# Kernel tuning notes

Measured on AMD Instinct MI355X. Metric: run time of the kernel, lower is better.

The kernel has to match this reference:

```python
import jax, jax.numpy as jnp
import numpy as np

SIGMA = 1.0
EPSILON = 1.0
MAX_ITER = 10


def pairwise_kernel(x, y, sigma=SIGMA):
    # k = -||x-y||^2 / (2 sigma^2), shape [B, L, K]
    outer = jnp.einsum('bld,bkd->blk', x, y)
    nx = jnp.sum(x * x, axis=2)
    ny = jnp.sum(y * y, axis=2)
    dist = jnp.clip(nx[:, :, None] + ny[:, None, :] - 2.0 * outer, 0.0, None)
    return -dist / (2.0 * sigma ** 2)


def c_transform(potential, log_weight, kernel, epsilon=EPSILON):
    # rho=None => scale=1, lse = -eps * logsumexp(kernel/eps + (pot/eps + log_w))
    s = potential / epsilon + log_weight            # [B, K]
    operand = kernel / epsilon + s[:, None, :]      # [B, L, K]
    return -epsilon * jax.scipy.special.logsumexp(operand, axis=2)


def potentials(kxy, log_a, log_b):
    kyx = jnp.swapaxes(kxy, 1, 2)
    f0 = jnp.zeros_like(log_a)
    g0 = jnp.zeros_like(log_b)

    def step(carry, _):
        f, g = carry
        fn = c_transform(g, log_b, kxy)
        gn = c_transform(f, log_a, kyx)
        return ((fn + f) * 0.5, (gn + g) * 0.5), None

    (f, g), _ = jax.lax.scan(step, (f0, g0), None, length=MAX_ITER)
    return f, g


def sym_potential(x, log_a):
    kxx = pairwise_kernel(x, x)
    f0 = jnp.zeros_like(log_a)

    def step(f, _):
        fn = c_transform(f, log_a, kxx)
        return (fn + f) * 0.5, None

    f, _ = jax.lax.scan(step, f0, None, length=MAX_ITER)
    return f


def evaluate_potential(x, a, y, b, g):
    # phi_transform is identity for rho=None; scaled_dot_prod forward = sum(a*f, dim=1)
    kxy = pairwise_kernel(x, y)
    f = c_transform(g, jnp.log(b), kxy)
    return jnp.sum(a * f, axis=1)


def setup_inputs() -> dict:
    key = jax.random.key(0)
    k1, k2, k3, k4 = jax.random.split(key, 4)
    B, L, K, D = 8, 2048, 2048, 32
    x = jax.random.normal(k1, (B, L, D), dtype=jnp.float32)
    y = jax.random.normal(k2, (B, K, D), dtype=jnp.float32)
    a = jax.random.uniform(k3, (B, L), dtype=jnp.float32, minval=0.1, maxval=1.0)
    b = jax.random.uniform(k4, (B, K), dtype=jnp.float32, minval=0.1, maxval=1.0)
    a = a / jnp.sum(a, axis=1, keepdims=True)
    b = b / jnp.sum(b, axis=1, keepdims=True)
    return {"x": x, "a": a, "y": y, "b": b}


def reference(x, a, y, b):
    log_a, log_b = jnp.log(a), jnp.log(b)
    kxy = pairwise_kernel(x, y)
    f, g = potentials(kxy, log_a, log_b)
    dist = evaluate_potential(x, a, y, b, g) + evaluate_potential(y, b, x, a, f)
    fx = sym_potential(x, log_a)
    fy = sym_potential(y, log_b)
    ent_x = evaluate_potential(x, a, x, a, fx)
    ent_y = evaluate_potential(y, b, y, b, fy)
    return jnp.mean(dist - ent_x - ent_y)
```

## Files before the change

### kernel.cpp

```cpp
#include <hip/hip_runtime.h>
#include <math.h>

#define BATCH 8
#define NPT   2048
#define DIM   32
#define RPB   64
#define CPW   (NPT / 4)
#define NT    (CPW / 16)
#define L2E   1.44269504088896f
#define BIAS2   96.0f
#define BIASLN  66.54212933375474f
#define BN    (BATCH * NPT)

typedef __attribute__((ext_vector_type(8))) _Float16 half8;
typedef __attribute__((ext_vector_type(4))) float floatx4;
typedef unsigned short u16;
typedef unsigned int u32;

__device__ __forceinline__ u16 f2h_bits(float v) {
    _Float16 h = (_Float16)v;
    return *(u16*)&h;
}
__device__ __forceinline__ float exp2v(float x) { return __builtin_amdgcn_exp2f(x); }

struct CtSet {
    const u16* Ah;
    const u16* Bh;
    const float* tls;
    const float* qX;
    const float* normR;
    const float* cn;
    const float* bmIn;
    const float* cwNext;
    const float* prev;
    float* out;
    float* tlsOut;
    float* bmOut;
};
struct CtArgs { CtSet s[4]; int average; };

__global__ __launch_bounds__(256, 4) void ct_kernel(CtArgs args) {
    const CtSet cs = args.s[blockIdx.y];
    const int batch = blockIdx.z;
    const int row0 = blockIdx.x * RPB;
    const int tid  = threadIdx.x;
    const int w = tid >> 6, lane = tid & 63, n = lane & 15, quad = lane >> 4;
    const int qk = quad * 8;
    const size_t pbase = (size_t)batch * NPT * DIM;
    const size_t vbase = (size_t)batch * NPT;

    __shared__ float lsum[RPB][4];

    const u16* __restrict__ Ah = cs.Ah + pbase;
    const u16* __restrict__ Bh = cs.Bh + pbase;
    const float* __restrict__ tls = cs.tls + vbase;

    half8 ah[4];
    #pragma unroll
    for (int s = 0; s < 4; s++) {
        size_t off = (size_t)(row0 + s * 16 + n) * DIM + qk;
        ah[s] = *(const half8*)(Ah + off);
    }

    float tmv = fmaxf(cs.bmIn[batch * 128 + lane], cs.bmIn[batch * 128 + 64 + lane]);
    #pragma unroll
    for (int m = 1; m < 64; m <<= 1) tmv = fmaxf(tmv, __shfl_xor(tmv, m, 64));
    const float Tmax = tmv;
    const float cnv = cs.cn[batch];

    float M0s[4][4];
    #pragma unroll
    for (int s = 0; s < 4; s++)
        #pragma unroll
        for (int r = 0; r < 4; r++) {
            int row = row0 + s * 16 + quad * 4 + r;
            M0s[s][r] = L2E * (cs.normR[vbase + row] * cnv + Tmax) - BIAS2;
        }

    float sum[4][4];
    #pragma unroll
    for (int s = 0; s < 4; s++)
        #pragma unroll
        for (int r = 0; r < 4; r++) sum[s][r] = 0.0f;

    const int c0 = w * CPW + n;
    const u16* bp = Bh + (size_t)c0 * DIM + qk;
    const float* tp = tls + c0;

    half8 b0, b1;
    float t0, t1;
    b0 = *(const half8*)bp;  t0 = *tp;

    #pragma unroll 1
    for (int ch = 0; ch < NT; ch += 2) {
        b1 = *(const half8*)(bp + (size_t)(ch + 1) * 16 * DIM);
        t1 = tp[(ch + 1) * 16];
        {
            floatx4 acc[4];
            #pragma unroll
            for (int s = 0; s < 4; s++)
                acc[s] = (floatx4){t0 - M0s[s][0], t0 - M0s[s][1],
                                   t0 - M0s[s][2], t0 - M0s[s][3]};
            #pragma unroll
            for (int s = 0; s < 4; s++)
                acc[s] = __builtin_amdgcn_mfma_f32_16x16x32_f16(ah[s], b0, acc[s], 0, 0, 0);
            #pragma unroll
            for (int s = 0; s < 4; s++)
                #pragma unroll
                for (int r = 0; r < 4; r++)
                    sum[s][r] += exp2v(acc[s][r]);
        }
        if (ch + 2 < NT) {
            b0 = *(const half8*)(bp + (size_t)(ch + 2) * 16 * DIM);
            t0 = tp[(ch + 2) * 16];
        }
        {
            floatx4 acc[4];
            #pragma unroll
            for (int s = 0; s < 4; s++)
                acc[s] = (floatx4){t1 - M0s[s][0], t1 - M0s[s][1],
                                   t1 - M0s[s][2], t1 - M0s[s][3]};
            #pragma unroll
            for (int s = 0; s < 4; s++)
                acc[s] = __builtin_amdgcn_mfma_f32_16x16x32_f16(ah[s], b1, acc[s], 0, 0, 0);
            #pragma unroll
            for (int s = 0; s < 4; s++)
                #pragma unroll
                for (int r = 0; r < 4; r++)
                    sum[s][r] += exp2v(acc[s][r]);
        }
    }

    #pragma unroll
    for (int s = 0; s < 4; s++)
        #pragma unroll
        for (int r = 0; r < 4; r++) {
            float v = sum[s][r];
            #pragma unroll
            for (int m = 1; m < 16; m <<= 1) v += __shfl_xor(v, m, 64);
            if (n == 0) lsum[s * 16 + quad * 4 + r][w] = v;
        }
    __syncthreads();

    if (tid < RPB) {
        float T = (lsum[tid][0] + lsum[tid][1]) + (lsum[tid][2] + lsum[tid][3]);
        int l = row0 + tid;
        float M0 = cs.normR[vbase + l] * cnv + Tmax;
        float lse = M0 + __logf(T) - BIASLN;
        float val = cs.qX[vbase + l] - lse;
        if (args.average) val = 0.5f * (cs.prev[vbase + l] + val);
        cs.out[vbase + l] = val;
        float tc = val + cs.cwNext[vbase + l];
        cs.tlsOut[vbase + l] = L2E * tc;
        float bm = tc;
        #pragma unroll
        for (int m = 1; m < 16; m <<= 1) bm = fmaxf(bm, __shfl_xor(bm, m, 64));
        if ((tid & 15) == 0)
            cs.bmOut[batch * 128 + blockIdx.x * 4 + (tid >> 4)] = bm;
    }
}

struct InitArgs {
    const float *x, *a, *y, *b;
    float *c_x, *c_y, *qx, *qy, *nx, *ny;
    u16 *xh, *yh, *xsh, *ysh;
    float *f0, *g0, *fx0, *fy0;
    float *tlsF0, *tlsG0, *tlsFx0, *tlsFy0;
    float *bmF0, *bmG0, *bmFx0, *bmFy0;
};

__global__ __launch_bounds__(256) void init_kernel(InitArgs ia) {
    int idx = blockIdx.x * 256 + threadIdx.x;
    if (idx >= BN) return;
    const float* xp = ia.x + (size_t)idx * DIM;
    const float* yp = ia.y + (size_t)idx * DIM;
    u32* xhp  = (u32*)ia.xh  + (size_t)idx * (DIM / 2);
    u32* yhp  = (u32*)ia.yh  + (size_t)idx * (DIM / 2);
    u32* xshp = (u32*)ia.xsh + (size_t)idx * (DIM / 2);
    u32* yshp = (u32*)ia.ysh + (size_t)idx * (DIM / 2);
    float sx = 0.f, sy = 0.f;
    #pragma unroll
    for (int d = 0; d < DIM; d += 2) {
        float v0 = xp[d], v1 = xp[d + 1];
        sx += v0 * v0 + v1 * v1;
        xhp[d / 2]  = (u32)f2h_bits(v0) | ((u32)f2h_bits(v1) << 16);
        xshp[d / 2] = (u32)f2h_bits(L2E * v0) | ((u32)f2h_bits(L2E * v1) << 16);
        float u0 = yp[d], u1 = yp[d + 1];
        sy += u0 * u0 + u1 * u1;
        yhp[d / 2]  = (u32)f2h_bits(u0) | ((u32)f2h_bits(u1) << 16);
        yshp[d / 2] = (u32)f2h_bits(L2E * u0) | ((u32)f2h_bits(L2E * u1) << 16);
    }
    float qxv = 0.5f * sx, qyv = 0.5f * sy;
    ia.qx[idx] = qxv; ia.qy[idx] = qyv;
    ia.nx[idx] = sqrtf(sx); ia.ny[idx] = sqrtf(sy);
    float cxv = __logf(ia.a[idx]) - qxv;
    float cyv = __logf(ia.b[idx]) - qyv;
    ia.c_x[idx] = cxv; ia.c_y[idx] = cyv;
    ia.f0[idx] = 0.f; ia.g0[idx] = 0.f; ia.fx0[idx] = 0.f; ia.fy0[idx] = 0.f;
    ia.tlsF0[idx] = L2E * cxv; ia.tlsG0[idx] = L2E * cyv;
    ia.tlsFx0[idx] = L2E * cxv; ia.tlsFy0[idx] = L2E * cyv;
    float mx = cxv, my = cyv;
    #pragma unroll
    for (int m = 1; m < 16; m <<= 1) {
        mx = fmaxf(mx, __shfl_xor(mx, m, 32));
        my = fmaxf(my, __shfl_xor(my, m, 32));
    }
    if ((threadIdx.x & 15) == 0) {
        int g = idx >> 4;
        ia.bmF0[g] = mx; ia.bmFx0[g] = mx;
        ia.bmG0[g] = my; ia.bmFy0[g] = my;
    }
}

__global__ __launch_bounds__(256) void precomp_kernel(const float* __restrict__ qx,
                                                      const float* __restrict__ qy,
                                                      float* __restrict__ cn) {
    int side = blockIdx.x, batch = blockIdx.y;
    const float* q = side ? qy : qx;
    float m = 0.f;
    for (int k = threadIdx.x; k < NPT; k += 256) m = fmaxf(m, q[(size_t)batch * NPT + k]);
    #pragma unroll
    for (int mm = 1; mm < 64; mm <<= 1) m = fmaxf(m, __shfl_xor(m, mm, 64));
    __shared__ float sm[4];
    if ((threadIdx.x & 63) == 0) sm[threadIdx.x >> 6] = m;
    __syncthreads();
    if (threadIdx.x == 0) {
        float v = fmaxf(fmaxf(sm[0], sm[1]), fmaxf(sm[2], sm[3]));
        cn[side * BATCH + batch] = sqrtf(2.f * v);
    }
}

__global__ __launch_bounds__(1024) void reduce_kernel(
        const float* __restrict__ a, const float* __restrict__ b,
        const float* __restrict__ ctA, const float* __restrict__ ctB,
        const float* __restrict__ ctX, const float* __restrict__ ctY,
        float* __restrict__ out) {
    float acc = 0.f;
    for (int idx = threadIdx.x; idx < BN; idx += 1024) {
        acc += a[idx] * (ctA[idx] - ctX[idx]) + b[idx] * (ctB[idx] - ctY[idx]);
    }
    #pragma unroll
    for (int off = 32; off > 0; off >>= 1) acc += __shfl_down(acc, off, 64);
    __shared__ float sm[16];
    if ((threadIdx.x & 63) == 0) sm[threadIdx.x >> 6] = acc;
    __syncthreads();
    if (threadIdx.x == 0) {
        float t = 0.f;
        #pragma unroll
        for (int i = 0; i < 16; i++) t += sm[i];
        out[0] = t / (float)BATCH;
    }
}

extern "C" void kernel_launch(void* const* d_in, const int* in_sizes, int n_in,
                              void* d_out, int out_size, void* d_ws, size_t ws_size,
                              hipStream_t stream) {
    const float* x = (const float*)d_in[0];
    const float* a = (const float*)d_in[1];
    const float* y = (const float*)d_in[2];
    const float* b = (const float*)d_in[3];
    float* out = (float*)d_out;

    float* ws = (float*)d_ws;
    float* c_x = ws + 0 * BN;
    float* c_y = ws + 1 * BN;
    float* qx  = ws + 2 * BN;
    float* qy  = ws + 3 * BN;
    float* nx  = ws + 4 * BN;
    float* ny  = ws + 5 * BN;
    float* fb[2]  = { ws + 6 * BN,  ws + 7 * BN };
    float* gb[2]  = { ws + 8 * BN,  ws + 9 * BN };
    float* fxb[2] = { ws + 10 * BN, ws + 11 * BN };
    float* fyb[2] = { ws + 12 * BN, ws + 13 * BN };
    float* ctA = ws + 14 * BN;
    float* ctB = ws + 15 * BN;
    float* ctX = ws + 16 * BN;
    float* ctY = ws + 17 * BN;
    float* tlsF[2]  = { ws + 18 * BN, ws + 19 * BN };
    float* tlsG[2]  = { ws + 20 * BN, ws + 21 * BN };
    float* tlsFx[2] = { ws + 22 * BN, ws + 23 * BN };
    float* tlsFy[2] = { ws + 24 * BN, ws + 25 * BN };
    float* dummyT = ws + 26 * BN;
    float* small = ws + 27 * BN;
    float* bmF[2]  = { small + 0 * 1024, small + 1 * 1024 };
    float* bmG[2]  = { small + 2 * 1024, small + 3 * 1024 };
    float* bmFx[2] = { small + 4 * 1024, small + 5 * 1024 };
    float* bmFy[2] = { small + 6 * 1024, small + 7 * 1024 };
    float* dummyB = small + 8 * 1024;
    float* cn = small + 9 * 1024;
    u16* bf = (u16*)(small + 10 * 1024);
    const size_t AS = (size_t)BN * DIM;
    u16* xh  = bf + 0 * AS;
    u16* yh  = bf + 1 * AS;
    u16* xsh = bf + 2 * AS;
    u16* ysh = bf + 3 * AS;

    InitArgs ia;
    ia.x = x; ia.a = a; ia.y = y; ia.b = b;
    ia.c_x = c_x; ia.c_y = c_y; ia.qx = qx; ia.qy = qy; ia.nx = nx; ia.ny = ny;
    ia.xh = xh; ia.yh = yh; ia.xsh = xsh; ia.ysh = ysh;
    ia.f0 = fb[0]; ia.g0 = gb[0]; ia.fx0 = fxb[0]; ia.fy0 = fyb[0];
    ia.tlsF0 = tlsF[0]; ia.tlsG0 = tlsG[0]; ia.tlsFx0 = tlsFx[0]; ia.tlsFy0 = tlsFy[0];
    ia.bmF0 = bmF[0]; ia.bmG0 = bmG[0]; ia.bmFx0 = bmFx[0]; ia.bmFy0 = bmFy[0];
    init_kernel<<<BN / 256, 256, 0, stream>>>(ia);
    precomp_kernel<<<dim3(2, BATCH), 256, 0, stream>>>(qx, qy, cn);

    dim3 grid(NPT / RPB, 4, BATCH);
    int cur = 0;
    for (int it = 0; it < 10; it++) {
        CtArgs ar;
        ar.average = 1;
        ar.s[0] = { xh, ysh, tlsG[cur], qx, nx, cn + BATCH, bmG[cur], c_x,
                    fb[cur], fb[1 - cur], tlsF[1 - cur], bmF[1 - cur] };
        ar.s[1] = { yh, xsh, tlsF[cur], qy, ny, cn, bmF[cur], c_y,
                    gb[cur], gb[1 - cur], tlsG[1 - cur], bmG[1 - cur] };
        ar.s[2] = { xh, xsh, tlsFx[cur], qx, nx, cn, bmFx[cur], c_x,
                    fxb[cur], fxb[1 - cur], tlsFx[1 - cur], bmFx[1 - cur] };
        ar.s[3] = { yh, ysh, tlsFy[cur], qy, ny, cn + BATCH, bmFy[cur], c_y,
                    fyb[cur], fyb[1 - cur], tlsFy[1 - cur], bmFy[1 - cur] };
        ct_kernel<<<grid, 256, 0, stream>>>(ar);
        cur ^= 1;
    }

    CtArgs fin;
    fin.average = 0;
    fin.s[0] = { xh, ysh, tlsG[cur], qx, nx, cn + BATCH, bmG[cur], c_x,
                 fb[cur], ctA, dummyT, dummyB };
    fin.s[1] = { yh, xsh, tlsF[cur], qy, ny, cn, bmF[cur], c_y,
                 gb[cur], ctB, dummyT, dummyB };
    fin.s[2] = { xh, xsh, tlsFx[cur], qx, nx, cn, bmFx[cur], c_x,
                 fxb[cur], ctX, dummyT, dummyB };
    fin.s[3] = { yh, ysh, tlsFy[cur], qy, ny, cn + BATCH, bmFy[cur], c_y,
                 fyb[cur], ctY, dummyT, dummyB };
    ct_kernel<<<grid, 256, 0, stream>>>(fin);

    reduce_kernel<<<1, 1024, 0, stream>>>(a, b, ctA, ctB, ctX, ctY, out);
}
```

Before: 338.2 us.

## Factor column weight out of exp, drop per-row bias, halve rows per block

Rewrites the logsumexp stabilisation. The per-column term is now computed once as a weight exp2(t - Tmax) and applied with an FMA to exp2 of the raw MFMA dot product, replacing the per-row norm-based bias seeded into the accumulator. This removes the normR/cn inputs, the precompute kernel and the per-row bias subtraction. Rows per block drop from 64 to 32 and launch bounds rise to 8 blocks per CU, which halves A-fragment reuse per B load but allows more occupancy. The change risks overflow or underflow in exp2 of the unbiased dot product and in the separately exponentiated weight, since the per-row max shift is gone.

```diff
diff --git a/kernel.cpp b/kernel.cpp
--- a/kernel.cpp
+++ b/kernel.cpp
@@ -4,12 +4,10 @@
 #define BATCH 8
 #define NPT   2048
 #define DIM   32
-#define RPB   64
+#define RPB   32
 #define CPW   (NPT / 4)
 #define NT    (CPW / 16)
 #define L2E   1.44269504088896f
-#define BIAS2   96.0f
-#define BIASLN  66.54212933375474f
 #define BN    (BATCH * NPT)
 
 typedef __attribute__((ext_vector_type(8))) _Float16 half8;
@@ -28,8 +26,6 @@
     const u16* Bh;
     const float* tls;
     const float* qX;
-    const float* normR;
-    const float* cn;
     const float* bmIn;
     const float* cwNext;
     const float* prev;
@@ -39,7 +35,7 @@
 };
 struct CtArgs { CtSet s[4]; int average; };
 
-__global__ __launch_bounds__(256, 4) void ct_kernel(CtArgs args) {
+__global__ __launch_bounds__(256, 8) void ct_kernel(CtArgs args) {
     const CtSet cs = args.s[blockIdx.y];
     const int batch = blockIdx.z;
     const int row0 = blockIdx.x * RPB;
@@ -55,9 +51,9 @@
     const u16* __restrict__ Bh = cs.Bh + pbase;
     const float* __restrict__ tls = cs.tls + vbase;
 
-    half8 ah[4];
-    #pragma unroll
-    for (int s = 0; s < 4; s++) {
+    half8 ah[2];
+    #pragma unroll
+    for (int s = 0; s < 2; s++) {
         size_t off = (size_t)(row0 + s * 16 + n) * DIM + qk;
         ah[s] = *(const half8*)(Ah + off);
     }
@@ -66,20 +62,11 @@
     #pragma unroll
     for (int m = 1; m < 64; m <<= 1) tmv = fmaxf(tmv, __shfl_xor(tmv, m, 64));
     const float Tmax = tmv;
-    const float cnv = cs.cn[batch];
-
-    float M0s[4][4];
-    #pragma unroll
-    for (int s = 0; s < 4; s++)
-        #pragma unroll
-        for (int r = 0; r < 4; r++) {
-            int row = row0 + s * 16 + quad * 4 + r;
-            M0s[s][r] = L2E * (cs.normR[vbase + row] * cnv + Tmax) - BIAS2;
-        }
-
-    float sum[4][4];
-    #pragma unroll
-    for (int s = 0; s < 4; s++)
+    const float l2eTmax = L2E * Tmax;
+
+    float sum[2][4];
+    #pragma unroll
+    for (int s = 0; s < 2; s++)
         #pragma unroll
         for (int r = 0; r < 4; r++) sum[s][r] = 0.0f;
 
@@ -96,43 +83,41 @@
         b1 = *(const half8*)(bp + (size_t)(ch + 1) * 16 * DIM);
         t1 = tp[(ch + 1) * 16];
         {
-            floatx4 acc[4];
-            #pragma unroll
-            for (int s = 0; s < 4; s++)
-                acc[s] = (floatx4){t0 - M0s[s][0], t0 - M0s[s][1],
-                                   t0 - M0s[s][2], t0 - M0s[s][3]};
-            #pragma unroll
-            for (int s = 0; s < 4; s++)
+            float wq = exp2v(t0 - l2eTmax);
+            floatx4 acc[2];
+            #pragma unroll
+            for (int s = 0; s < 2; s++) acc[s] = (floatx4){0.f, 0.f, 0.f, 0.f};
+            #pragma unroll
+            for (int s = 0; s < 2; s++)
                 acc[s] = __builtin_amdgcn_mfma_f32_16x16x32_f16(ah[s], b0, acc[s], 0, 0, 0);
             #pragma unroll
-            for (int s = 0; s < 4; s++)
+            for (int s = 0; s < 2; s++)
                 #pragma unroll
                 for (int r = 0; r < 4; r++)
-                    sum[s][r] += exp2v(acc[s][r]);
+                    sum[s][r] = fmaf(wq, exp2v(acc[s][r]), sum[s][r]);
         }
         if (ch + 2 < NT) {
             b0 = *(const half8*)(bp + (size_t)(ch + 2) * 16 * DIM);
             t0 = tp[(ch + 2) * 16];
         }
         {
-            floatx4 acc[4];
-            #pragma unroll
-            for (int s = 0; s < 4; s++)
-                acc[s] = (floatx4){t1 - M0s[s][0], t1 - M0s[s][1],
-                                   t1 - M0s[s][2], t1 - M0s[s][3]};
-            #pragma unroll
-            for (int s = 0; s < 4; s++)
+            float wq = exp2v(t1 - l2eTmax);
+            floatx4 acc[2];
+            #pragma unroll
+            for (int s = 0; s < 2; s++) acc[s] = (floatx4){0.f, 0.f, 0.f, 0.f};
+            #pragma unroll
+            for (int s = 0; s < 2; s++)
                 acc[s] = __builtin_amdgcn_mfma_f32_16x16x32_f16(ah[s], b1, acc[s], 0, 0, 0);
             #pragma unroll
-            for (int s = 0; s < 4; s++)
+            for (int s = 0; s < 2; s++)
                 #pragma unroll
                 for (int r = 0; r < 4; r++)
-                    sum[s][r] += exp2v(acc[s][r]);
-        }
-    }
-
-    #pragma unroll
-    for (int s = 0; s < 4; s++)
+                    sum[s][r] = fmaf(wq, exp2v(acc[s][r]), sum[s][r]);
+        }
+    }
+
+    #pragma unroll
+    for (int s = 0; s < 2; s++)
         #pragma unroll
         for (int r = 0; r < 4; r++) {
             float v = sum[s][r];
@@ -145,8 +130,7 @@
     if (tid < RPB) {
         float T = (lsum[tid][0] + lsum[tid][1]) + (lsum[tid][2] + lsum[tid][3]);
         int l = row0 + tid;
-        float M0 = cs.normR[vbase + l] * cnv + Tmax;
-        float lse = M0 + __logf(T) - BIASLN;
+        float lse = Tmax + __logf(T);
         float val = cs.qX[vbase + l] - lse;
         if (args.average) val = 0.5f * (cs.prev[vbase + l] + val);
         cs.out[vbase + l] = val;
@@ -156,13 +140,13 @@
         #pragma unroll
         for (int m = 1; m < 16; m <<= 1) bm = fmaxf(bm, __shfl_xor(bm, m, 64));
         if ((tid & 15) == 0)
-            cs.bmOut[batch * 128 + blockIdx.x * 4 + (tid >> 4)] = bm;
+            cs.bmOut[batch * 128 + blockIdx.x * 2 + (tid >> 4)] = bm;
     }
 }
 
 struct InitArgs {
     const float *x, *a, *y, *b;
-    float *c_x, *c_y, *qx, *qy, *nx, *ny;
+    float *c_x, *c_y, *qx, *qy;
     u16 *xh, *yh, *xsh, *ysh;
     float *f0, *g0, *fx0, *fy0;
     float *tlsF0, *tlsG0, *tlsFx0, *tlsFy0;
@@ -192,7 +176,6 @@
     }
     float qxv = 0.5f * sx, qyv = 0.5f * sy;
     ia.qx[idx] = qxv; ia.qy[idx] = qyv;
-    ia.nx[idx] = sqrtf(sx); ia.ny[idx] = sqrtf(sy);
     float cxv = __logf(ia.a[idx]) - qxv;
     float cyv = __logf(ia.b[idx]) - qyv;
     ia.c_x[idx] = cxv; ia.c_y[idx] = cyv;
@@ -209,24 +192,6 @@
         int g = idx >> 4;
         ia.bmF0[g] = mx; ia.bmFx0[g] = mx;
         ia.bmG0[g] = my; ia.bmFy0[g] = my;
-    }
-}
-
-__global__ __launch_bounds__(256) void precomp_kernel(const float* __restrict__ qx,
-                                                      const float* __restrict__ qy,
-                                                      float* __restrict__ cn) {
-    int side = blockIdx.x, batch = blockIdx.y;
-    const float* q = side ? qy : qx;
-    float m = 0.f;
-    for (int k = threadIdx.x; k < NPT; k += 256) m = fmaxf(m, q[(size_t)batch * NPT + k]);
-    #pragma unroll
-    for (int mm = 1; mm < 64; mm <<= 1) m = fmaxf(m, __shfl_xor(m, mm, 64));
-    __shared__ float sm[4];
-    if ((threadIdx.x & 63) == 0) sm[threadIdx.x >> 6] = m;
-    __syncthreads();
-    if (threadIdx.x == 0) {
-        float v = fmaxf(fmaxf(sm[0], sm[1]), fmaxf(sm[2], sm[3]));
-        cn[side * BATCH + batch] = sqrtf(2.f * v);
     }
 }
 
@@ -266,28 +231,25 @@
     float* c_y = ws + 1 * BN;
     float* qx  = ws + 2 * BN;
     float* qy  = ws + 3 * BN;
-    float* nx  = ws + 4 * BN;
-    float* ny  = ws + 5 * BN;
-    float* fb[2]  = { ws + 6 * BN,  ws + 7 * BN };
-    float* gb[2]  = { ws + 8 * BN,  ws + 9 * BN };
-    float* fxb[2] = { ws + 10 * BN, ws + 11 * BN };
-    float* fyb[2] = { ws + 12 * BN, ws + 13 * BN };
-    float* ctA = ws + 14 * BN;
-    float* ctB = ws + 15 * BN;
-    float* ctX = ws + 16 * BN;
-    float* ctY = ws + 17 * BN;
-    float* tlsF[2]  = { ws + 18 * BN, ws + 19 * BN };
-    float* tlsG[2]  = { ws + 20 * BN, ws + 21 * BN };
-    float* tlsFx[2] = { ws + 22 * BN, ws + 23 * BN };
-    float* tlsFy[2] = { ws + 24 * BN, ws + 25 * BN };
-    float* dummyT = ws + 26 * BN;
-    float* small = ws + 27 * BN;
+    float* fb[2]  = { ws + 4 * BN,  ws + 5 * BN };
+    float* gb[2]  = { ws + 6 * BN,  ws + 7 * BN };
+    float* fxb[2] = { ws + 8 * BN,  ws + 9 * BN };
+    float* fyb[2] = { ws + 10 * BN, ws + 11 * BN };
+    float* ctA = ws + 12 * BN;
+    float* ctB = ws + 13 * BN;
+    float* ctX = ws + 14 * BN;
+    float* ctY = ws + 15 * BN;
+    float* tlsF[2]  = { ws + 16 * BN, ws + 17 * BN };
+    float* tlsG[2]  = { ws + 18 * BN, ws + 19 * BN };
+    float* tlsFx[2] = { ws + 20 * BN, ws + 21 * BN };
+    float* tlsFy[2] = { ws + 22 * BN, ws + 23 * BN };
+    float* dummyT = ws + 24 * BN;
+    float* small = ws + 25 * BN;
     float* bmF[2]  = { small + 0 * 1024, small + 1 * 1024 };
     float* bmG[2]  = { small + 2 * 1024, small + 3 * 1024 };
     float* bmFx[2] = { small + 4 * 1024, small + 5 * 1024 };
     float* bmFy[2] = { small + 6 * 1024, small + 7 * 1024 };
     float* dummyB = small + 8 * 1024;
-    float* cn = small + 9 * 1024;
     u16* bf = (u16*)(small + 10 * 1024);
     const size_t AS = (size_t)BN * DIM;
     u16* xh  = bf + 0 * AS;
@@ -297,26 +259,25 @@
 
     InitArgs ia;
     ia.x = x; ia.a = a; ia.y = y; ia.b = b;
-    ia.c_x = c_x; ia.c_y = c_y; ia.qx = qx; ia.qy = qy; ia.nx = nx; ia.ny = ny;
+    ia.c_x = c_x; ia.c_y = c_y; ia.qx = qx; ia.qy = qy;
     ia.xh = xh; ia.yh = yh; ia.xsh = xsh; ia.ysh = ysh;
     ia.f0 = fb[0]; ia.g0 = gb[0]; ia.fx0 = fxb[0]; ia.fy0 = fyb[0];
     ia.tlsF0 = tlsF[0]; ia.tlsG0 = tlsG[0]; ia.tlsFx0 = tlsFx[0]; ia.tlsFy0 = tlsFy[0];
     ia.bmF0 = bmF[0]; ia.bmG0 = bmG[0]; ia.bmFx0 = bmFx[0]; ia.bmFy0 = bmFy[0];
     init_kernel<<<BN / 256, 256, 0, stream>>>(ia);
-    precomp_kernel<<<dim3(2, BATCH), 256, 0, stream>>>(qx, qy, cn);
 
     dim3 grid(NPT / RPB, 4, BATCH);
     int cur = 0;
     for (int it = 0; it < 10; it++) {
         CtArgs ar;
         ar.average = 1;
-        ar.s[0] = { xh, ysh, tlsG[cur], qx, nx, cn + BATCH, bmG[cur], c_x,
+        ar.s[0] = { xh, ysh, tlsG[cur], qx, bmG[cur], c_x,
                     fb[cur], fb[1 - cur], tlsF[1 - cur], bmF[1 - cur] };
-        ar.s[1] = { yh, xsh, tlsF[cur], qy, ny, cn, bmF[cur], c_y,
+        ar.s[1] = { yh, xsh, tlsF[cur], qy, bmF[cur], c_y,
                     gb[cur], gb[1 - cur], tlsG[1 - cur], bmG[1 - cur] };
-        ar.s[2] = { xh, xsh, tlsFx[cur], qx, nx, cn, bmFx[cur], c_x,
+        ar.s[2] = { xh, xsh, tlsFx[cur], qx, bmFx[cur], c_x,
                     fxb[cur], fxb[1 - cur], tlsFx[1 - cur], bmFx[1 - cur] };
-        ar.s[3] = { yh, ysh, tlsFy[cur], qy, ny, cn + BATCH, bmFy[cur], c_y,
+        ar.s[3] = { yh, ysh, tlsFy[cur], qy, bmFy[cur], c_y,
                     fyb[cur], fyb[1 - cur], tlsFy[1 - cur], bmFy[1 - cur] };
         ct_kernel<<<grid, 256, 0, stream>>>(ar);
         cur ^= 1;
@@ -324,14 +285,10 @@
 
     CtArgs fin;
     fin.average = 0;
-    fin.s[0] = { xh, ysh, tlsG[cur], qx, nx, cn + BATCH, bmG[cur], c_x,
-                 fb[cur], ctA, dummyT, dummyB };
-    fin.s[1] = { yh, xsh, tlsF[cur], qy, ny, cn, bmF[cur], c_y,
-                 gb[cur], ctB, dummyT, dummyB };
-    fin.s[2] = { xh, xsh, tlsFx[cur], qx, nx, cn, bmFx[cur], c_x,
-                 fxb[cur], ctX, dummyT, dummyB };
-    fin.s[3] = { yh, ysh, tlsFy[cur], qy, ny, cn + BATCH, bmFy[cur], c_y,
-                 fyb[cur], ctY, dummyT, dummyB };
+    fin.s[0] = { xh, ysh, tlsG[cur], qx, bmG[cur], c_x, fb[cur], ctA, dummyT, dummyB };
+    fin.s[1] = { yh, xsh, tlsF[cur], qy, bmF[cur], c_y, gb[cur], ctB, dummyT, dummyB };
+    fin.s[2] = { xh, xsh, tlsFx[cur], qx, bmFx[cur], c_x, fxb[cur], ctX, dummyT, dummyB };
+    fin.s[3] = { yh, ysh, tlsFy[cur], qy, bmFy[cur], c_y, fyb[cur], ctY, dummyT, dummyB };
     ct_kernel<<<grid, 256, 0, stream>>>(fin);
 
     reduce_kernel<<<1, 1024, 0, stream>>>(a, b, ctA, ctB, ctX, ctY, out);
```

After: 327.6 us. -3.1%, faster.
